# Kernel tuning notes

Hardware: AMD Instinct MI355X
Metric: run time of the kernel (lower is better)

The kernel has to match this reference:

```python
import jax, jax.numpy as jnp
import numpy as np

TREND_SCALING = 0.6
DETAIL_PRESERVATION = 0.85
SPIKE_THRESHOLD = 3.5
SPIKE_DAMPING = 0.35
ITERATIONS = 2
EPS = 1e-6


def _smooth(x, kernel):
    # x: [B, C, L], kernel: [1, 1, W] (normalized box filter)
    W = kernel.shape[-1]
    pad = W // 2
    xp = jnp.pad(x, ((0, 0), (0, 0), (pad, pad)), mode='reflect')
    C = x.shape[1]
    w = jnp.broadcast_to(kernel, (C, 1, W))  # depthwise weight [C, 1, W]
    return jax.lax.conv_general_dilated(
        xp, w, window_strides=(1,), padding='VALID',
        dimension_numbers=('NCH', 'OIH', 'NCH'), feature_group_count=C)


def setup_inputs() -> dict:
    key = jax.random.key(0)
    x = jax.random.normal(key, (16, 32, 65536), dtype=jnp.float32)
    # buffers from __init__ with base_window=5
    detail_kernel = jnp.ones((1, 1, 5), dtype=jnp.float32) / 5.0
    trend_kernel = jnp.ones((1, 1, 11), dtype=jnp.float32) / 11.0
    return {"x": x, "detail_kernel": detail_kernel, "trend_kernel": trend_kernel}


def reference(x, detail_kernel, trend_kernel):
    current = x.astype(jnp.float32)
    for _ in range(ITERATIONS):
        trend = _smooth(current, trend_kernel)
        local = _smooth(current, detail_kernel)
        residual = current - local
        # torch .std uses Bessel's correction (ddof=1)
        scale = jnp.maximum(jnp.std(residual, axis=-1, keepdims=True, ddof=1), EPS)
        threshold = scale * SPIKE_THRESHOLD
        residual = jnp.where(jnp.abs(residual) > threshold,
                             residual * SPIKE_DAMPING, residual)
        residual = residual * DETAIL_PRESERVATION
        combined = (1.0 - TREND_SCALING) * local + TREND_SCALING * trend
        current = combined + residual
    return current
```

## Files before the change

### kernel.cpp

```cpp
#include <hip/hip_runtime.h>
#include <math.h>


#define LROW  65536
#define NROWS 512
#define NT    256
#define TPE   8
#define EPB   (NT * TPE)
#define BPR   (LROW / EPB)
#define GRID  (NROWS * BPR)
#define WPB   (NT / 64)
#define PPR   (BPR * WPB)

#define TS 0.6f
#define DP 0.85f
#define SD 0.35f

typedef float floatx4 __attribute__((ext_vector_type(4)));

__device__ __forceinline__ int refl(int g) {
    return g < 0 ? -g : (g >= LROW ? 2 * LROW - 2 - g : g);
}

__device__ __forceinline__ void wave_reduce_store(double s, double q, int tid,
                                                  int bid, double2* parts) {
#pragma unroll
    for (int off = 32; off; off >>= 1) {
        s += __shfl_down(s, off);
        q += __shfl_down(q, off);
    }
    if ((tid & 63) == 0) {
        double2 v; v.x = s; v.y = q;
        parts[(size_t)bid * WPB + (tid >> 6)] = v;
    }
}

__global__ __launch_bounds__(NT) void k_stats1(const float* __restrict__ x,
                                               const float* __restrict__ k5p,
                                               double2* __restrict__ parts) {
    const int bid = blockIdx.x, tid = threadIdx.x;
    const int row = bid / BPR, ck = bid % BPR;
    const float* rp = x + (size_t)row * LROW;
    const int t = ck * EPB + tid * TPE;
    const float w5 = k5p[0];

    float f[16];
    if (t >= 4 && t + 12 <= LROW) {
        const float4* p4 = (const float4*)(rp + t - 4);
#pragma unroll
        for (int i = 0; i < 4; i++) {
            float4 u = p4[i];
            f[4 * i] = u.x; f[4 * i + 1] = u.y; f[4 * i + 2] = u.z; f[4 * i + 3] = u.w;
        }
    } else {
#pragma unroll
        for (int i = 0; i < 16; i++) f[i] = rp[refl(t - 4 + i)];
    }

    double s = 0.0, q = 0.0;
#pragma unroll
    for (int k = 0; k < TPE; k++) {
        float loc = 0.f;
#pragma unroll
        for (int d = 0; d < 5; d++) loc = fmaf(f[k + 2 + d], w5, loc);
        float r = f[k + 4] - loc;
        s += (double)r;
        q += (double)r * (double)r;
    }
    wave_reduce_store(s, q, tid, bid, parts);
}

__global__ void k_thr(const double2* __restrict__ parts, float* __restrict__ th) {
    int r = blockIdx.x * blockDim.x + threadIdx.x;
    if (r >= NROWS) return;
    const double2* p = parts + (size_t)r * PPR;
    double S = 0.0, Q = 0.0;
    for (int i = 0; i < PPR; i++) { S += p[i].x; Q += p[i].y; }
    const double N = (double)LROW;
    double var = (Q - S * S / N) / (N - 1.0);
    if (var < 0.0) var = 0.0;
    th[r] = fmaxf((float)sqrt(var), 1e-6f) * 3.5f;
}

__global__ __launch_bounds__(NT) void k_apply1(const float* __restrict__ x,
                                               float* __restrict__ cur2,
                                               const float* __restrict__ k5p,
                                               const float* __restrict__ k11p,
                                               const float* __restrict__ th1,
                                               double2* __restrict__ parts2) {
    const int bid = blockIdx.x, tid = threadIdx.x;
    const int row = bid / BPR, ck = bid % BPR;
    const float* rp = x + (size_t)row * LROW;
    const int t = ck * EPB + tid * TPE;
    const float w5 = k5p[0], w11 = k11p[0], th = th1[row];

    float f[24];
    if (t >= 8 && t + 16 <= LROW) {
        const float4* p4 = (const float4*)(rp + t - 8);
#pragma unroll
        for (int i = 0; i < 6; i++) {
            float4 u = p4[i];
            f[4 * i] = u.x; f[4 * i + 1] = u.y; f[4 * i + 2] = u.z; f[4 * i + 3] = u.w;
        }
    } else {
#pragma unroll
        for (int i = 0; i < 24; i++) f[i] = rp[refl(t - 8 + i)];
    }

    float c2[12];
#pragma unroll
    for (int j = 0; j < 12; j++) {
        float trend = 0.f, loc = 0.f;
#pragma unroll
        for (int d = 0; d < 11; d++) trend = fmaf(f[j + 1 + d], w11, trend);
#pragma unroll
        for (int d = 0; d < 5; d++) loc = fmaf(f[j + 4 + d], w5, loc);
        float r = f[j + 6] - loc;
        r = (fabsf(r) > th) ? r * SD : r;
        c2[j] = (1.0f - TS) * loc + TS * trend + DP * r;
    }

    double s = 0.0, q = 0.0;
#pragma unroll
    for (int k = 0; k < TPE; k++) {
        float loc = 0.f;
#pragma unroll
        for (int d = 0; d < 5; d++) loc = fmaf(c2[k + d], w5, loc);
        float r = c2[k + 2] - loc;
        s += (double)r;
        q += (double)r * (double)r;
    }

    float* op = cur2 + (size_t)row * LROW + t;
    ((float4*)op)[0] = make_float4(c2[2], c2[3], c2[4], c2[5]);
    ((float4*)op)[1] = make_float4(c2[6], c2[7], c2[8], c2[9]);

    wave_reduce_store(s, q, tid, bid, parts2);
}

__global__ __launch_bounds__(NT) void k_apply2(const float* __restrict__ cur2,
                                               float* __restrict__ out,
                                               const float* __restrict__ k5p,
                                               const float* __restrict__ k11p,
                                               const float* __restrict__ th2) {
    const int bid = blockIdx.x, tid = threadIdx.x;
    const int row = bid / BPR, ck = bid % BPR;
    const float* rp = cur2 + (size_t)row * LROW;
    const int t = ck * EPB + tid * TPE;
    const float w5 = k5p[0], w11 = k11p[0], th = th2[row];

    float f[24];
    if (t >= 8 && t + 16 <= LROW) {
        const float4* p4 = (const float4*)(rp + t - 8);
#pragma unroll
        for (int i = 0; i < 6; i++) {
            float4 u = p4[i];
            f[4 * i] = u.x; f[4 * i + 1] = u.y; f[4 * i + 2] = u.z; f[4 * i + 3] = u.w;
        }
    } else {
#pragma unroll
        for (int i = 0; i < 24; i++) f[i] = rp[refl(t - 8 + i)];
    }

    float o[TPE];
#pragma unroll
    for (int k = 0; k < TPE; k++) {
        float trend = 0.f, loc = 0.f;
#pragma unroll
        for (int d = 0; d < 11; d++) trend = fmaf(f[k + 3 + d], w11, trend);
#pragma unroll
        for (int d = 0; d < 5; d++) loc = fmaf(f[k + 6 + d], w5, loc);
        float r = f[k + 8] - loc;
        r = (fabsf(r) > th) ? r * SD : r;
        o[k] = (1.0f - TS) * loc + TS * trend + DP * r;
    }

    floatx4* op = (floatx4*)(out + (size_t)row * LROW + t);
    floatx4 v0 = { o[0], o[1], o[2], o[3] };
    floatx4 v1 = { o[4], o[5], o[6], o[7] };
    __builtin_nontemporal_store(v0, op);
    __builtin_nontemporal_store(v1, op + 1);
}

extern "C" void kernel_launch(void* const* d_in, const int* in_sizes, int n_in,
                              void* d_out, int out_size, void* d_ws, size_t ws_size,
                              hipStream_t stream) {
    const float* x   = (const float*)d_in[0];
    const float* k5  = (const float*)d_in[1];
    const float* k11 = (const float*)d_in[2];
    float* out = (float*)d_out;

    float*   cur2 = (float*)d_ws;
    double2* p1   = (double2*)((char*)d_ws + (size_t)LROW * NROWS * 4);
    double2* p2   = p1 + (size_t)GRID * WPB;
    float*   th1  = (float*)(p2 + (size_t)GRID * WPB);
    float*   th2  = th1 + NROWS;

    hipLaunchKernelGGL(k_stats1, dim3(GRID), dim3(NT), 0, stream, x, k5, p1);
    hipLaunchKernelGGL(k_thr, dim3(1), dim3(NROWS), 0, stream, p1, th1);
    hipLaunchKernelGGL(k_apply1, dim3(GRID), dim3(NT), 0, stream,
                       x, cur2, k5, k11, th1, p2);
    hipLaunchKernelGGL(k_thr, dim3(1), dim3(NROWS), 0, stream, p2, th2);
    hipLaunchKernelGGL(k_apply2, dim3(GRID), dim3(NT), 0, stream,
                       cur2, out, k5, k11, th2);
}
```

Baseline: 363.6 us.

## Recompute first iteration in final pass instead of storing intermediate; parallelize threshold reduction

```diff
diff --git a/kernel.cpp b/kernel.cpp
--- a/kernel.cpp
+++ b/kernel.cpp
@@ -70,20 +70,26 @@
     wave_reduce_store(s, q, tid, bid, parts);
 }
 
-__global__ void k_thr(const double2* __restrict__ parts, float* __restrict__ th) {
-    int r = blockIdx.x * blockDim.x + threadIdx.x;
-    if (r >= NROWS) return;
+__global__ __launch_bounds__(64) void k_thr(const double2* __restrict__ parts,
+                                            float* __restrict__ th) {
+    const int r = blockIdx.x, lane = threadIdx.x;
     const double2* p = parts + (size_t)r * PPR;
-    double S = 0.0, Q = 0.0;
-    for (int i = 0; i < PPR; i++) { S += p[i].x; Q += p[i].y; }
-    const double N = (double)LROW;
-    double var = (Q - S * S / N) / (N - 1.0);
-    if (var < 0.0) var = 0.0;
-    th[r] = fmaxf((float)sqrt(var), 1e-6f) * 3.5f;
-}
-
-__global__ __launch_bounds__(NT) void k_apply1(const float* __restrict__ x,
-                                               float* __restrict__ cur2,
+    double2 a = p[lane], b = p[lane + 64];
+    double s = a.x + b.x, q = a.y + b.y;
+#pragma unroll
+    for (int off = 32; off; off >>= 1) {
+        s += __shfl_down(s, off);
+        q += __shfl_down(q, off);
+    }
+    if (lane == 0) {
+        const double N = (double)LROW;
+        double var = (q - s * s / N) / (N - 1.0);
+        if (var < 0.0) var = 0.0;
+        th[r] = fmaxf((float)sqrt(var), 1e-6f) * 3.5f;
+    }
+}
+
+__global__ __launch_bounds__(NT) void k_stats2(const float* __restrict__ x,
                                                const float* __restrict__ k5p,
                                                const float* __restrict__ k11p,
                                                const float* __restrict__ th1,
@@ -130,36 +136,46 @@
         s += (double)r;
         q += (double)r * (double)r;
     }
-
-    float* op = cur2 + (size_t)row * LROW + t;
-    ((float4*)op)[0] = make_float4(c2[2], c2[3], c2[4], c2[5]);
-    ((float4*)op)[1] = make_float4(c2[6], c2[7], c2[8], c2[9]);
-
     wave_reduce_store(s, q, tid, bid, parts2);
 }
 
-__global__ __launch_bounds__(NT) void k_apply2(const float* __restrict__ cur2,
-                                               float* __restrict__ out,
-                                               const float* __restrict__ k5p,
-                                               const float* __restrict__ k11p,
-                                               const float* __restrict__ th2) {
+__global__ __launch_bounds__(NT) void k_final(const float* __restrict__ x,
+                                              float* __restrict__ out,
+                                              const float* __restrict__ k5p,
+                                              const float* __restrict__ k11p,
+                                              const float* __restrict__ th1,
+                                              const float* __restrict__ th2) {
     const int bid = blockIdx.x, tid = threadIdx.x;
     const int row = bid / BPR, ck = bid % BPR;
-    const float* rp = cur2 + (size_t)row * LROW;
+    const float* rp = x + (size_t)row * LROW;
     const int t = ck * EPB + tid * TPE;
-    const float w5 = k5p[0], w11 = k11p[0], th = th2[row];
-
-    float f[24];
-    if (t >= 8 && t + 16 <= LROW) {
-        const float4* p4 = (const float4*)(rp + t - 8);
-#pragma unroll
-        for (int i = 0; i < 6; i++) {
+    const float w5 = k5p[0], w11 = k11p[0];
+    const float tA = th1[row], tB = th2[row];
+
+    float f[40];
+    if (t >= 16 && t + 24 <= LROW) {
+        const float4* p4 = (const float4*)(rp + t - 16);
+#pragma unroll
+        for (int i = 0; i < 10; i++) {
             float4 u = p4[i];
             f[4 * i] = u.x; f[4 * i + 1] = u.y; f[4 * i + 2] = u.z; f[4 * i + 3] = u.w;
         }
     } else {
 #pragma unroll
-        for (int i = 0; i < 24; i++) f[i] = rp[refl(t - 8 + i)];
+        for (int i = 0; i < 40; i++) f[i] = rp[refl(t - 16 + i)];
+    }
+
+    float c2[24];
+#pragma unroll
+    for (int j = 0; j < 24; j++) {
+        float trend = 0.f, loc = 0.f;
+#pragma unroll
+        for (int d = 0; d < 11; d++) trend = fmaf(f[j + 3 + d], w11, trend);
+#pragma unroll
+        for (int d = 0; d < 5; d++) loc = fmaf(f[j + 6 + d], w5, loc);
+        float r = f[j + 8] - loc;
+        r = (fabsf(r) > tA) ? r * SD : r;
+        c2[j] = (1.0f - TS) * loc + TS * trend + DP * r;
     }
 
     float o[TPE];
@@ -167,11 +183,11 @@
     for (int k = 0; k < TPE; k++) {
         float trend = 0.f, loc = 0.f;
 #pragma unroll
-        for (int d = 0; d < 11; d++) trend = fmaf(f[k + 3 + d], w11, trend);
-#pragma unroll
-        for (int d = 0; d < 5; d++) loc = fmaf(f[k + 6 + d], w5, loc);
-        float r = f[k + 8] - loc;
-        r = (fabsf(r) > th) ? r * SD : r;
+        for (int d = 0; d < 11; d++) trend = fmaf(c2[k + 3 + d], w11, trend);
+#pragma unroll
+        for (int d = 0; d < 5; d++) loc = fmaf(c2[k + 6 + d], w5, loc);
+        float r = c2[k + 8] - loc;
+        r = (fabsf(r) > tB) ? r * SD : r;
         o[k] = (1.0f - TS) * loc + TS * trend + DP * r;
     }
 
@@ -190,17 +206,16 @@
     const float* k11 = (const float*)d_in[2];
     float* out = (float*)d_out;
 
-    float*   cur2 = (float*)d_ws;
-    double2* p1   = (double2*)((char*)d_ws + (size_t)LROW * NROWS * 4);
-    double2* p2   = p1 + (size_t)GRID * WPB;
-    float*   th1  = (float*)(p2 + (size_t)GRID * WPB);
-    float*   th2  = th1 + NROWS;
+    double2* p1  = (double2*)d_ws;
+    double2* p2  = p1 + (size_t)GRID * WPB;
+    float*   th1 = (float*)(p2 + (size_t)GRID * WPB);
+    float*   th2 = th1 + NROWS;
 
     hipLaunchKernelGGL(k_stats1, dim3(GRID), dim3(NT), 0, stream, x, k5, p1);
-    hipLaunchKernelGGL(k_thr, dim3(1), dim3(NROWS), 0, stream, p1, th1);
-    hipLaunchKernelGGL(k_apply1, dim3(GRID), dim3(NT), 0, stream,
-                       x, cur2, k5, k11, th1, p2);
-    hipLaunchKernelGGL(k_thr, dim3(1), dim3(NROWS), 0, stream, p2, th2);
-    hipLaunchKernelGGL(k_apply2, dim3(GRID), dim3(NT), 0, stream,
-                       cur2, out, k5, k11, th2);
-}
+    hipLaunchKernelGGL(k_thr, dim3(NROWS), dim3(64), 0, stream, p1, th1);
+    hipLaunchKernelGGL(k_stats2, dim3(GRID), dim3(NT), 0, stream,
+                       x, k5, k11, th1, p2);
+    hipLaunchKernelGGL(k_thr, dim3(NROWS), dim3(64), 0, stream, p2, th2);
+    hipLaunchKernelGGL(k_final, dim3(GRID), dim3(NT), 0, stream,
+                       x, out, k5, k11, th1, th2);
+}
```

Measured after the change: 455.2 us. 25.2% more time.
